# Performance work log

Measured on AMD Instinct MI355X. Metric: run time of the kernel, lower is better.

The kernel has to match this reference:

```python
import jax, jax.numpy as jnp
import numpy as np

L, N = 200, 256  # event_list_length, num_nodes


def setup_inputs() -> dict:
    key = jax.random.key(0)
    ks = jax.random.split(key, 7)
    time = jax.random.uniform(ks[0], (2,), dtype=jnp.float32)
    event_list = jax.random.normal(ks[1], (L + 1, N, N), dtype=jnp.float32)
    u_begin = jax.random.uniform(ks[2], (N, N, 3), dtype=jnp.float32)
    # xavier-ish scales for params
    a = jax.random.normal(ks[3], (L, N, N, 3), dtype=jnp.float32) * 0.05
    w = jax.random.normal(ks[4], (L, N, 1, N), dtype=jnp.float32) * 0.05
    liner_w = jax.random.normal(ks[5], (N, 3), dtype=jnp.float32) * 0.5
    liner_b = jax.random.normal(ks[6], (N,), dtype=jnp.float32) * 0.1
    return {"time": time, "event_list": event_list, "u_begin": u_begin,
            "a": a, "w": w, "liner_w": liner_w, "liner_b": liner_b,
            "batch_size": 2}


def reference(time, event_list, u_begin, a, w, liner_w, liner_b, batch_size):
    # event_list[:-1]; consumed in pairs (start, start+1) with batch_size == 2
    T = event_list.shape[0] - 1
    S = T // batch_size                      # number of scan steps
    n = event_list.shape[1]
    e2 = event_list[:T].reshape(S, 2, n, n)          # [S,2,N,N]
    a2 = a[:T].reshape(S, 2, n, n, 3)                # [S,2,N,N,3]
    w2 = w[:T, :, 0, :].reshape(S, 2, n, n)          # [S,2,N,N] (squeeze the 1-dim)
    t0, t1 = time[0], time[1]                        # original always uses time[0], time[1]

    def step(u, xs):
        ep, ap, wp = xs                              # [2,N,N], [2,N,N,3], [2,N,N]
        # per-node scalar dot: w[start][node] @ event_begin[k][node]
        dot0 = jnp.einsum('nk,nk->n', wp[0], ep[0])  # [N]
        dot1 = jnp.einsum('nk,nk->n', wp[1], ep[1])
        # math.exp in the original returns a Python float -> constant w.r.t. autograd
        f0 = jax.lax.stop_gradient(jnp.exp(-dot0 * t0))[:, None, None]
        f1 = jax.lax.stop_gradient(jnp.exp(-dot1 * t1))[:, None, None]
        lamda = u + ap[0] * f0 + ap[1] * f1          # [N,N,3]
        temp = jax.nn.softmax(lamda, axis=-1)        # softmax over the 3-dim (dim=1 of [N,3] per node)
        # per-node Linear(3,1): temp[node] @ W_node^T + b_node -> [N,N]
        out = jnp.einsum('nmc,nc->nm', temp, liner_w) + liner_b[:, None]
        # state update was .detach().cpu().numpy() -> stop_gradient
        return jax.lax.stop_gradient(temp), out

    _, outs = jax.lax.scan(step, u_begin, (e2, a2, w2))
    return outs                                      # [S, N, N] == [T/2, N, N]
```

## Files before the change

### kernel.cpp

```cpp
#include <hip/hip_runtime.h>


#define NN   256
#define TT   200
#define SS   100
#define DD   10
#define NG   (SS / DD)

__global__ __launch_bounds__(256) void fused_scan_kernel(
    const float* __restrict__ timep,
    const float* __restrict__ ev,
    const float* __restrict__ ub,
    const float* __restrict__ a,
    const float* __restrict__ w,
    const float* __restrict__ lw,
    const float* __restrict__ lb,
    float* __restrict__ out)
{
    __shared__ float2 fs2[SS];
    float* fsbuf = (float*)fs2;

    const int n    = blockIdx.x;
    const int m    = threadIdx.x;
    const int lane = m & 63;
    const int wid  = m >> 6;

    const size_t TSTRIDE = (size_t)NN * NN * 3;
    const size_t base    = (size_t)n * (NN * 3) + (size_t)m * 3;

    float rg[DD][6];
    const float* pf = a + base;
    {
#pragma unroll
        for (int j = 0; j < DD; ++j) {
            rg[j][0] = pf[0];
            rg[j][1] = pf[1];
            rg[j][2] = pf[2];
            rg[j][3] = pf[TSTRIDE + 0];
            rg[j][4] = pf[TSTRIDE + 1];
            rg[j][5] = pf[TSTRIDE + 2];
            pf += 2 * TSTRIDE;
        }
    }
    asm volatile("" ::: "memory");

    const float t0 = timep[0];
    const float t1 = timep[1];
    const float tsel = (wid & 1) ? t1 : t0;

    {
        const size_t rowoff = (size_t)n * NN;
        const float* wrow = w  + rowoff;
        const float* erow = ev + rowoff;
#pragma unroll 2
        for (int t = wid; t < TT; t += 20) {
            float d[5];
#pragma unroll
            for (int q = 0; q < 5; ++q) {
                const int tq = t + 4 * q;
                float4 wv = ((const float4*)(wrow + (size_t)tq * (NN * NN)))[lane];
                float4 evv = ((const float4*)(erow + (size_t)tq * (NN * NN)))[lane];
                float dq = wv.x * evv.x;
                dq = fmaf(wv.y, evv.y, dq);
                dq = fmaf(wv.z, evv.z, dq);
                dq = fmaf(wv.w, evv.w, dq);
                d[q] = dq;
            }
#pragma unroll
            for (int off = 1; off < 64; off <<= 1) {
#pragma unroll
                for (int q = 0; q < 5; ++q)
                    d[q] += __shfl_xor(d[q], off, 64);
            }
            if (lane == 0) {
#pragma unroll
                for (int q = 0; q < 5; ++q)
                    fsbuf[t + 4 * q] = __expf(-d[q] * tsel);
            }
        }
    }

    const float w0 = lw[n * 3 + 0];
    const float w1 = lw[n * 3 + 1];
    const float w2 = lw[n * 3 + 2];
    const float bb = lb[n];

    float u0 = ub[base + 0];
    float u1 = ub[base + 1];
    float u2 = ub[base + 2];

    __syncthreads();

    float* op = out + (size_t)n * NN + m;

    for (int g = 0; g < NG - 1; ++g) {
        const int sb = g * DD;
#pragma unroll
        for (int j = 0; j < DD; ++j) {
            const int s = sb + j;
            const float2 ff = fs2[s];
            float l0 = fmaf(rg[j][0], ff.x, fmaf(rg[j][3], ff.y, u0));
            float l1 = fmaf(rg[j][1], ff.x, fmaf(rg[j][4], ff.y, u1));
            float l2 = fmaf(rg[j][2], ff.x, fmaf(rg[j][5], ff.y, u2));
            rg[j][0] = pf[0];
            rg[j][1] = pf[1];
            rg[j][2] = pf[2];
            rg[j][3] = pf[TSTRIDE + 0];
            rg[j][4] = pf[TSTRIDE + 1];
            rg[j][5] = pf[TSTRIDE + 2];
            pf += 2 * TSTRIDE;
            float mx  = fmaxf(l0, fmaxf(l1, l2));
            float e0  = __expf(l0 - mx);
            float e1  = __expf(l1 - mx);
            float e2  = __expf(l2 - mx);
            float inv = __builtin_amdgcn_rcpf(e0 + e1 + e2);
            u0 = e0 * inv;
            u1 = e1 * inv;
            u2 = e2 * inv;
            __builtin_nontemporal_store(
                fmaf(u0, w0, fmaf(u1, w1, fmaf(u2, w2, bb))),
                op + (size_t)s * (NN * NN));
        }
    }
    {
        const int sb = (NG - 1) * DD;
#pragma unroll
        for (int j = 0; j < DD; ++j) {
            const int s = sb + j;
            const float2 ff = fs2[s];
            float l0 = fmaf(rg[j][0], ff.x, fmaf(rg[j][3], ff.y, u0));
            float l1 = fmaf(rg[j][1], ff.x, fmaf(rg[j][4], ff.y, u1));
            float l2 = fmaf(rg[j][2], ff.x, fmaf(rg[j][5], ff.y, u2));
            float mx  = fmaxf(l0, fmaxf(l1, l2));
            float e0  = __expf(l0 - mx);
            float e1  = __expf(l1 - mx);
            float e2  = __expf(l2 - mx);
            float inv = __builtin_amdgcn_rcpf(e0 + e1 + e2);
            u0 = e0 * inv;
            u1 = e1 * inv;
            u2 = e2 * inv;
            __builtin_nontemporal_store(
                fmaf(u0, w0, fmaf(u1, w1, fmaf(u2, w2, bb))),
                op + (size_t)s * (NN * NN));
        }
    }
}

extern "C" void kernel_launch(void* const* d_in, const int* in_sizes, int n_in,
                              void* d_out, int out_size, void* d_ws, size_t ws_size,
                              hipStream_t stream) {
    const float* timep = (const float*)d_in[0];
    const float* ev    = (const float*)d_in[1];
    const float* ub    = (const float*)d_in[2];
    const float* a     = (const float*)d_in[3];
    const float* w     = (const float*)d_in[4];
    const float* lw    = (const float*)d_in[5];
    const float* lb    = (const float*)d_in[6];
    float* out = (float*)d_out;

    fused_scan_kernel<<<NN, 256, 0, stream>>>(timep, ev, ub, a, w, lw, lb, out);
}
```

Measured before the change: 307.1 us.

## Split exp-factor precompute into separate kernel and spread scan loads across quad threads

The per-node dot products and exponentials move into their own kernel, which runs one wavefront per (time, node) row and writes to a workspace. The scan kernel then launches four times as many blocks. Each chain is handled by four lanes, and each lane loads one of four consecutive `a` slices. Lane shuffles combine the slices, and every lane redundantly runs the two softmax steps per iteration. This targets the latency-bound streaming of `a` with only 256 blocks. The cost is an extra launch, a workspace round trip and quadrupled softmax arithmetic.

```diff
diff --git a/kernel.cpp b/kernel.cpp
--- a/kernel.cpp
+++ b/kernel.cpp
@@ -5,143 +5,141 @@
 #define TT   200
 #define SS   100
 #define DD   10
-#define NG   (SS / DD)
+#define NG   (50 / DD)
 
-__global__ __launch_bounds__(256) void fused_scan_kernel(
+__global__ __launch_bounds__(256) void f_kernel(
     const float* __restrict__ timep,
     const float* __restrict__ ev,
+    const float* __restrict__ w,
+    float* __restrict__ fws)
+{
+    const int tid  = threadIdx.x;
+    const int lane = tid & 63;
+    const int row  = blockIdx.x * 4 + (tid >> 6);
+    const int t    = row >> 8;
+    const int n    = row & 255;
+
+    const size_t off = (size_t)t * (NN * NN) + (size_t)n * NN;
+    const float4 wv  = ((const float4*)(w  + off))[lane];
+    const float4 evv = ((const float4*)(ev + off))[lane];
+
+    float d = wv.x * evv.x;
+    d = fmaf(wv.y, evv.y, d);
+    d = fmaf(wv.z, evv.z, d);
+    d = fmaf(wv.w, evv.w, d);
+#pragma unroll
+    for (int off2 = 1; off2 < 64; off2 <<= 1)
+        d += __shfl_xor(d, off2, 64);
+
+    if (lane == 0) {
+        const float tsel = (t & 1) ? timep[1] : timep[0];
+        fws[n * TT + t] = __expf(-d * tsel);
+    }
+}
+
+__global__ __launch_bounds__(256, 4) void scan_kernel(
+    const float* __restrict__ fws,
     const float* __restrict__ ub,
     const float* __restrict__ a,
-    const float* __restrict__ w,
     const float* __restrict__ lw,
     const float* __restrict__ lb,
     float* __restrict__ out)
 {
-    __shared__ float2 fs2[SS];
-    float* fsbuf = (float*)fs2;
+    __shared__ float fs[TT];
 
     const int n    = blockIdx.x;
-    const int m    = threadIdx.x;
-    const int lane = m & 63;
-    const int wid  = m >> 6;
+    const int qtr  = blockIdx.y;
+    const int tid  = threadIdx.x;
+    const int sub  = tid & 3;
+    const int par  = sub >> 1;
+    const int chain = qtr * 64 + (tid >> 2);
 
-    const size_t TSTRIDE = (size_t)NN * NN * 3;
-    const size_t base    = (size_t)n * (NN * 3) + (size_t)m * 3;
+    if (tid < TT) fs[tid] = fws[n * TT + tid];
 
-    float rg[DD][6];
-    const float* pf = a + base;
-    {
-#pragma unroll
-        for (int j = 0; j < DD; ++j) {
-            rg[j][0] = pf[0];
-            rg[j][1] = pf[1];
-            rg[j][2] = pf[2];
-            rg[j][3] = pf[TSTRIDE + 0];
-            rg[j][4] = pf[TSTRIDE + 1];
-            rg[j][5] = pf[TSTRIDE + 2];
-            pf += 2 * TSTRIDE;
-        }
-    }
-    asm volatile("" ::: "memory");
+    const size_t TS    = (size_t)NN * NN * 3;
+    const size_t cbase = (size_t)n * (NN * 3) + (size_t)chain * 3;
 
-    const float t0 = timep[0];
-    const float t1 = timep[1];
-    const float tsel = (wid & 1) ? t1 : t0;
-
-    {
-        const size_t rowoff = (size_t)n * NN;
-        const float* wrow = w  + rowoff;
-        const float* erow = ev + rowoff;
-#pragma unroll 2
-        for (int t = wid; t < TT; t += 20) {
-            float d[5];
-#pragma unroll
-            for (int q = 0; q < 5; ++q) {
-                const int tq = t + 4 * q;
-                float4 wv = ((const float4*)(wrow + (size_t)tq * (NN * NN)))[lane];
-                float4 evv = ((const float4*)(erow + (size_t)tq * (NN * NN)))[lane];
-                float dq = wv.x * evv.x;
-                dq = fmaf(wv.y, evv.y, dq);
-                dq = fmaf(wv.z, evv.z, dq);
-                dq = fmaf(wv.w, evv.w, dq);
-                d[q] = dq;
-            }
-#pragma unroll
-            for (int off = 1; off < 64; off <<= 1) {
-#pragma unroll
-                for (int q = 0; q < 5; ++q)
-                    d[q] += __shfl_xor(d[q], off, 64);
-            }
-            if (lane == 0) {
-#pragma unroll
-                for (int q = 0; q < 5; ++q)
-                    fsbuf[t + 4 * q] = __expf(-d[q] * tsel);
-            }
-        }
-    }
-
+    float u0 = ub[cbase + 0];
+    float u1 = ub[cbase + 1];
+    float u2 = ub[cbase + 2];
     const float w0 = lw[n * 3 + 0];
     const float w1 = lw[n * 3 + 1];
     const float w2 = lw[n * 3 + 2];
     const float bb = lb[n];
 
-    float u0 = ub[base + 0];
-    float u1 = ub[base + 1];
-    float u2 = ub[base + 2];
-
     __syncthreads();
 
-    float* op = out + (size_t)n * NN + m;
+    const float* pf = a + (size_t)sub * TS + cbase;
+    float rg[DD][3];
+#pragma unroll
+    for (int j = 0; j < DD; ++j) {
+        rg[j][0] = pf[0];
+        rg[j][1] = pf[1];
+        rg[j][2] = pf[2];
+        pf += 4 * TS;
+    }
 
-    for (int g = 0; g < NG - 1; ++g) {
-        const int sb = g * DD;
+    float* op = out + (size_t)n * NN + chain;
+    const bool sel = (par == 0);
+    const bool st  = (sub == 0);
+
+    for (int g = 0; g < NG; ++g) {
+        const int kb = g * DD;
 #pragma unroll
         for (int j = 0; j < DD; ++j) {
-            const int s = sb + j;
-            const float2 ff = fs2[s];
-            float l0 = fmaf(rg[j][0], ff.x, fmaf(rg[j][3], ff.y, u0));
-            float l1 = fmaf(rg[j][1], ff.x, fmaf(rg[j][4], ff.y, u1));
-            float l2 = fmaf(rg[j][2], ff.x, fmaf(rg[j][5], ff.y, u2));
-            rg[j][0] = pf[0];
-            rg[j][1] = pf[1];
-            rg[j][2] = pf[2];
-            rg[j][3] = pf[TSTRIDE + 0];
-            rg[j][4] = pf[TSTRIDE + 1];
-            rg[j][5] = pf[TSTRIDE + 2];
-            pf += 2 * TSTRIDE;
-            float mx  = fmaxf(l0, fmaxf(l1, l2));
-            float e0  = __expf(l0 - mx);
-            float e1  = __expf(l1 - mx);
-            float e2  = __expf(l2 - mx);
-            float inv = __builtin_amdgcn_rcpf(e0 + e1 + e2);
-            u0 = e0 * inv;
-            u1 = e1 * inv;
-            u2 = e2 * inv;
-            __builtin_nontemporal_store(
-                fmaf(u0, w0, fmaf(u1, w1, fmaf(u2, w2, bb))),
-                op + (size_t)s * (NN * NN));
-        }
-    }
-    {
-        const int sb = (NG - 1) * DD;
-#pragma unroll
-        for (int j = 0; j < DD; ++j) {
-            const int s = sb + j;
-            const float2 ff = fs2[s];
-            float l0 = fmaf(rg[j][0], ff.x, fmaf(rg[j][3], ff.y, u0));
-            float l1 = fmaf(rg[j][1], ff.x, fmaf(rg[j][4], ff.y, u1));
-            float l2 = fmaf(rg[j][2], ff.x, fmaf(rg[j][5], ff.y, u2));
-            float mx  = fmaxf(l0, fmaxf(l1, l2));
-            float e0  = __expf(l0 - mx);
-            float e1  = __expf(l1 - mx);
-            float e2  = __expf(l2 - mx);
-            float inv = __builtin_amdgcn_rcpf(e0 + e1 + e2);
-            u0 = e0 * inv;
-            u1 = e1 * inv;
-            u2 = e2 * inv;
-            __builtin_nontemporal_store(
-                fmaf(u0, w0, fmaf(u1, w1, fmaf(u2, w2, bb))),
-                op + (size_t)s * (NN * NN));
+            const int k = kb + j;
+            const float ff = fs[4 * k + sub];
+            float v0 = rg[j][0] * ff;
+            float v1 = rg[j][1] * ff;
+            float v2 = rg[j][2] * ff;
+            if (g != NG - 1) {
+                rg[j][0] = pf[0];
+                rg[j][1] = pf[1];
+                rg[j][2] = pf[2];
+                pf += 4 * TS;
+            }
+            float vv0 = v0 + __shfl_xor(v0, 1, 64);
+            float vv1 = v1 + __shfl_xor(v1, 1, 64);
+            float vv2 = v2 + __shfl_xor(v2, 1, 64);
+            float b0 = __shfl_xor(vv0, 2, 64);
+            float b1 = __shfl_xor(vv1, 2, 64);
+            float b2 = __shfl_xor(vv2, 2, 64);
+            {
+                float l0 = u0 + (sel ? vv0 : b0);
+                float l1 = u1 + (sel ? vv1 : b1);
+                float l2 = u2 + (sel ? vv2 : b2);
+                float mx  = fmaxf(l0, fmaxf(l1, l2));
+                float e0  = __expf(l0 - mx);
+                float e1  = __expf(l1 - mx);
+                float e2  = __expf(l2 - mx);
+                float inv = __builtin_amdgcn_rcpf(e0 + e1 + e2);
+                u0 = e0 * inv;
+                u1 = e1 * inv;
+                u2 = e2 * inv;
+                if (st) {
+                    __builtin_nontemporal_store(
+                        fmaf(u0, w0, fmaf(u1, w1, fmaf(u2, w2, bb))),
+                        op + (size_t)(2 * k) * (NN * NN));
+                }
+            }
+            {
+                float l0 = u0 + (sel ? b0 : vv0);
+                float l1 = u1 + (sel ? b1 : vv1);
+                float l2 = u2 + (sel ? b2 : vv2);
+                float mx  = fmaxf(l0, fmaxf(l1, l2));
+                float e0  = __expf(l0 - mx);
+                float e1  = __expf(l1 - mx);
+                float e2  = __expf(l2 - mx);
+                float inv = __builtin_amdgcn_rcpf(e0 + e1 + e2);
+                u0 = e0 * inv;
+                u1 = e1 * inv;
+                u2 = e2 * inv;
+                if (st) {
+                    __builtin_nontemporal_store(
+                        fmaf(u0, w0, fmaf(u1, w1, fmaf(u2, w2, bb))),
+                        op + (size_t)(2 * k + 1) * (NN * NN));
+                }
+            }
         }
     }
 }
@@ -157,6 +155,8 @@
     const float* lw    = (const float*)d_in[5];
     const float* lb    = (const float*)d_in[6];
     float* out = (float*)d_out;
+    float* fws = (float*)d_ws;
 
-    fused_scan_kernel<<<NN, 256, 0, stream>>>(timep, ev, ub, a, w, lw, lb, out);
+    f_kernel<<<(TT * NN) / 4, 256, 0, stream>>>(timep, ev, w, fws);
+    scan_kernel<<<dim3(NN, 4), 256, 0, stream>>>(fws, ub, a, lw, lb, out);
 }
```

After: 316.1 us. +3.0%, slower.
